# Kernel tuning notes

Hardware: AMD Instinct MI355X
Metric: run time of the kernel (lower is better)

Reference implementation:

```python
import jax, jax.numpy as jnp
import numpy as np

N, E, F = 50000, 1_600_000, 128
EPS = 1e-5
DATASET_NUM = 1.0


def _glorot(k, shape):
    lim = jnp.sqrt(6.0 / (shape[0] + shape[1]))
    return jax.random.uniform(k, shape, jnp.float32, -lim, lim)


def setup_inputs() -> dict:
    key = jax.random.key(0)
    ks = jax.random.split(key, 24)
    inp = {
        "x": jax.random.normal(ks[0], (N, F), jnp.float32),
        "noise": jax.random.normal(ks[1], (N, F), jnp.float32),
        "edge_index": jax.random.randint(ks[2], (2, E), 0, N, jnp.int64),
        # ChebConv K=2 weights: W0 (T_0 = x term), W1 (T_1 = L_hat x term)
        "W1_0": _glorot(ks[3], (F, 64)),  "W1_1": _glorot(ks[4], (F, 64)),  "b1": jnp.zeros((64,), jnp.float32),
        "g1": jnp.ones((64,), jnp.float32), "be1": jnp.zeros((64,), jnp.float32),
        "W2_0": _glorot(ks[5], (64, 16)), "W2_1": _glorot(ks[6], (64, 16)), "b2": jnp.zeros((16,), jnp.float32),
        "W3_0": _glorot(ks[7], (16, 64)), "W3_1": _glorot(ks[8], (16, 64)), "b3": jnp.zeros((64,), jnp.float32),
        "g3": jnp.ones((64,), jnp.float32), "be3": jnp.zeros((64,), jnp.float32),
        "W4_0": _glorot(ks[9], (64, F)),  "W4_1": _glorot(ks[10], (64, F)), "b4": jnp.zeros((F,), jnp.float32),
    }
    return inp


def reference(x, noise, edge_index, W1_0, W1_1, b1, g1, be1,
              W2_0, W2_1, b2, W3_0, W3_1, b3, g3, be3, W4_0, W4_1, b4):
    src, dst = edge_index[0], edge_index[1]
    n = x.shape[0]

    # train-mode noise injection: x + dataset_num * randn * x.mean()
    x = x + DATASET_NUM * noise * jnp.mean(x)

    # symmetric normalization; with lambda_max=2 the scaled Laplacian is -A_norm
    deg = jax.ops.segment_sum(jnp.ones_like(src, dtype=x.dtype), dst, num_segments=n)
    dinv = jnp.where(deg > 0, jax.lax.rsqrt(jnp.maximum(deg, 1.0)), 0.0)
    w_e = dinv[src] * dinv[dst]  # [E]

    def cheb(h, W0, W1, b):
        # T_0 = h ; T_1 = L_hat h = -A_norm h  (K=2 ChebConv)
        tx1 = -jax.ops.segment_sum(w_e[:, None] * h[src], dst, num_segments=n)
        return h @ W0 + tx1 @ W1 + b

    def bn(h, g, be):
        mu = jnp.mean(h, axis=0)
        var = jnp.mean((h - mu) ** 2, axis=0)
        return g * (h - mu) * jax.lax.rsqrt(var + EPS) + be

    h1 = jax.nn.relu(bn(cheb(x, W1_0, W1_1, b1), g1, be1))
    h2 = cheb(h1, W2_0, W2_1, b2)
    h3 = jax.nn.relu(bn(cheb(h2, W3_0, W3_1, b3), g3, be3))
    return cheb(h3, W4_0, W4_1, b4)
```

## Files before the change

### kernel.cpp

```cpp
#include <hip/hip_runtime.h>

#define NNODES 50000
#define NEDGES 1600000
#define FEAT   128
#define EPSV   1e-5f

__global__ __launch_bounds__(256) void sum_kernel(const float* __restrict__ x,
                                                  float* __restrict__ out, int n4) {
  const float4* x4 = (const float4*)x;
  float s = 0.f;
  for (int i = blockIdx.x * blockDim.x + threadIdx.x; i < n4; i += gridDim.x * blockDim.x) {
    float4 v = x4[i];
    s += v.x + v.y + v.z + v.w;
  }
  for (int off = 32; off > 0; off >>= 1) s += __shfl_down(s, off);
  __shared__ float ls[4];
  int wid = threadIdx.x >> 6;
  if ((threadIdx.x & 63) == 0) ls[wid] = s;
  __syncthreads();
  if (threadIdx.x == 0) atomicAdd(out, ls[0] + ls[1] + ls[2] + ls[3]);
}

__global__ __launch_bounds__(256) void noisy_kernel(const float* __restrict__ x,
                                                    const float* __restrict__ noise,
                                                    const float* __restrict__ sumv,
                                                    float* __restrict__ xn, int n4) {
  int i = blockIdx.x * blockDim.x + threadIdx.x;
  if (i >= n4) return;
  float mean = *sumv * (1.0f / (float)(NNODES * FEAT));
  float4 a = ((const float4*)x)[i];
  float4 b = ((const float4*)noise)[i];
  float4 o;
  o.x = a.x + b.x * mean; o.y = a.y + b.y * mean;
  o.z = a.z + b.z * mean; o.w = a.w + b.w * mean;
  ((float4*)xn)[i] = o;
}

__global__ __launch_bounds__(256) void degree_kernel(const int* __restrict__ ei,
                                                     int* __restrict__ degi, int ne) {
  int e = blockIdx.x * blockDim.x + threadIdx.x;
  if (e < ne) atomicAdd(&degi[ei[NEDGES + e]], 1);
}

__global__ __launch_bounds__(256) void dinv_kernel(const int* __restrict__ degi,
                                                   float* __restrict__ dinv, int n) {
  int i = blockIdx.x * blockDim.x + threadIdx.x;
  if (i < n) dinv[i] = (degi[i] > 0) ? rsqrtf((float)degi[i]) : 0.f;
}

__global__ __launch_bounds__(1024) void scan1_kernel(const int* __restrict__ cnt,
                                                     int* __restrict__ exc,
                                                     int* __restrict__ bsum, int n) {
  __shared__ int s[1024];
  int tid = threadIdx.x;
  int i = blockIdx.x * 1024 + tid;
  int v = (i < n) ? cnt[i] : 0;
  int val = v;
  s[tid] = v;
  __syncthreads();
  for (int off = 1; off < 1024; off <<= 1) {
    int t = (tid >= off) ? s[tid - off] : 0;
    __syncthreads();
    val += t;
    s[tid] = val;
    __syncthreads();
  }
  if (i < n) exc[i] = val - v;
  if (tid == 1023) bsum[blockIdx.x] = val;
}

__global__ __launch_bounds__(256) void scan2_kernel(int* __restrict__ bsum, int nb) {
  __shared__ int s[256];
  int tid = threadIdx.x;
  int v = (tid < nb) ? bsum[tid] : 0;
  int val = v;
  s[tid] = v;
  __syncthreads();
  for (int off = 1; off < 256; off <<= 1) {
    int t = (tid >= off) ? s[tid - off] : 0;
    __syncthreads();
    val += t;
    s[tid] = val;
    __syncthreads();
  }
  if (tid < nb) bsum[tid] = val - v;
}

__global__ __launch_bounds__(256) void scan3_kernel(int* __restrict__ row_ptr,
                                                    const int* __restrict__ bsum,
                                                    int* __restrict__ cursor, int n) {
  int i = blockIdx.x * blockDim.x + threadIdx.x;
  if (i < n) {
    int v = row_ptr[i] + bsum[i >> 10];
    row_ptr[i] = v;
    cursor[i] = v;
  } else if (i == n) {
    row_ptr[n] = NEDGES;
  }
}

__global__ __launch_bounds__(256) void csr_fill_kernel(const int* __restrict__ ei,
                                                       const float* __restrict__ dinv,
                                                       int* __restrict__ cursor,
                                                       int2* __restrict__ ep, int ne) {
  int e = blockIdx.x * blockDim.x + threadIdx.x;
  if (e >= ne) return;
  int s = ei[e];
  int d = ei[NEDGES + e];
  float w = dinv[s] * dinv[d];
  int pos = atomicAdd(&cursor[d], 1);
  ep[pos] = make_int2(s, __float_as_int(w));
}

template <int K, int NOUT, bool ROWCAT, bool BIAS>
__global__ __launch_bounds__(256) void gemm_kernel(const float* __restrict__ A1,
                                                   const float* __restrict__ A2,
                                                   const float* __restrict__ W0,
                                                   const float* __restrict__ W1,
                                                   const float* __restrict__ bias,
                                                   float* __restrict__ out, int n) {
  constexpr int TC  = NOUT / 4;
  constexpr int RG  = 256 / TC;
  constexpr int RPT = 4;
  constexpr int RPB = RG * RPT;
  constexpr int AP  = (K == 128) ? K : (K + 1);
  __shared__ float wl[K * NOUT];
  __shared__ float al[RPB * AP];
  const int tid = threadIdx.x;

  for (int i = tid; i < K * NOUT; i += 256) {
    int k = i / NOUT, j = i - k * NOUT;
    float v;
    if (ROWCAT) v = (k < K / 2) ? W0[k * NOUT + j] : W1[(k - K / 2) * NOUT + j];
    else        v = (j < NOUT / 2) ? W0[k * (NOUT / 2) + j] : W1[k * (NOUT / 2) + (j - NOUT / 2)];
    wl[i] = v;
  }
  const int row0 = blockIdx.x * RPB;
  for (int i = tid; i < RPB * K; i += 256) {
    int r = i / K, k = i - r * K;
    int gr = row0 + r;
    float v = 0.f;
    if (gr < n) {
      if (ROWCAT) v = (k < K / 2) ? A1[gr * (K / 2) + k] : A2[gr * (K / 2) + (k - K / 2)];
      else        v = A1[gr * K + k];
    }
    al[r * AP + k] = v;
  }
  __syncthreads();

  const int jt = (tid % TC) * 4;
  const int rbase = (tid / TC) * RPT;
  float acc[RPT][4] = {};
#pragma unroll 4
  for (int k = 0; k < K; ++k) {
    float4 w4 = *(const float4*)&wl[k * NOUT + jt];
#pragma unroll
    for (int rr = 0; rr < RPT; ++rr) {
      float a = al[(rbase + rr) * AP + k];
      acc[rr][0] = fmaf(a, w4.x, acc[rr][0]);
      acc[rr][1] = fmaf(a, w4.y, acc[rr][1]);
      acc[rr][2] = fmaf(a, w4.z, acc[rr][2]);
      acc[rr][3] = fmaf(a, w4.w, acc[rr][3]);
    }
  }
  float4 b4 = make_float4(0.f, 0.f, 0.f, 0.f);
  if (BIAS) b4 = *(const float4*)&bias[jt];
#pragma unroll
  for (int rr = 0; rr < RPT; ++rr) {
    int gr = row0 + rbase + rr;
    if (gr < n) {
      float4 o;
      o.x = acc[rr][0] + b4.x; o.y = acc[rr][1] + b4.y;
      o.z = acc[rr][2] + b4.z; o.w = acc[rr][3] + b4.w;
      *(float4*)&out[gr * NOUT + jt] = o;
    }
  }
}

template <int F, bool ADD>
__global__ __launch_bounds__(256) void spmm_kernel(const int* __restrict__ row_ptr,
                                                   const int2* __restrict__ ep,
                                                   const float* __restrict__ mat, int S, int OFF,
                                                   const float* __restrict__ bias,
                                                   float* __restrict__ out, int n) {
  constexpr int GP = 256 / F;
  const int f = threadIdx.x & (F - 1);
  const int g = threadIdx.x / F;
  const int node = blockIdx.x * GP + g;
  if (node >= n) return;
  const int beg = row_ptr[node];
  const int end = row_ptr[node + 1];
  float acc = 0.f;
  int e = beg;
  for (; e + 1 < end; e += 2) {
    int2 sw0 = ep[e];
    int2 sw1 = ep[e + 1];
    acc -= __int_as_float(sw0.y) * mat[sw0.x * S + OFF + f];
    acc -= __int_as_float(sw1.y) * mat[sw1.x * S + OFF + f];
  }
  if (e < end) {
    int2 sw = ep[e];
    acc -= __int_as_float(sw.y) * mat[sw.x * S + OFF + f];
  }
  float r = acc;
  if (ADD) r += mat[node * S + f] + bias[f];
  out[node * F + f] = r;
}

template <int F>
__global__ __launch_bounds__(256) void bn_stats_kernel(const float* __restrict__ z,
                                                       float* __restrict__ stats, int n) {
  __shared__ float s[2 * F];
  if (threadIdx.x < 2 * F) s[threadIdx.x] = 0.f;
  __syncthreads();
  constexpr int GP = 256 / F;
  const int f = threadIdx.x & (F - 1);
  const int g = threadIdx.x / F;
  float sum = 0.f, sq = 0.f;
  for (int r = blockIdx.x * GP + g; r < n; r += gridDim.x * GP) {
    float v = z[r * F + f];
    sum += v;
    sq += v * v;
  }
  atomicAdd(&s[f], sum);
  atomicAdd(&s[F + f], sq);
  __syncthreads();
  if (threadIdx.x < 2 * F) atomicAdd(&stats[threadIdx.x], s[threadIdx.x]);
}

template <int F>
__global__ __launch_bounds__(256) void bn_apply_kernel(float* __restrict__ z,
                                                       const float* __restrict__ stats,
                                                       const float* __restrict__ gw,
                                                       const float* __restrict__ be, int n) {
  const int idx = blockIdx.x * blockDim.x + threadIdx.x;
  if (idx >= n * F) return;
  const int f = idx & (F - 1);
  const float inv_n = 1.0f / (float)n;
  float mu = stats[f] * inv_n;
  float var = stats[F + f] * inv_n - mu * mu;
  float v = (z[idx] - mu) * rsqrtf(var + EPSV) * gw[f] + be[f];
  z[idx] = fmaxf(v, 0.f);
}

extern "C" void kernel_launch(void* const* d_in, const int* in_sizes, int n_in,
                              void* d_out, int out_size, void* d_ws, size_t ws_size,
                              hipStream_t stream) {
  const float* x     = (const float*)d_in[0];
  const float* noise = (const float*)d_in[1];
  const int*   ei    = (const int*)d_in[2];
  const float* W1_0 = (const float*)d_in[3];
  const float* W1_1 = (const float*)d_in[4];
  const float* b1   = (const float*)d_in[5];
  const float* g1   = (const float*)d_in[6];
  const float* be1  = (const float*)d_in[7];
  const float* W2_0 = (const float*)d_in[8];
  const float* W2_1 = (const float*)d_in[9];
  const float* b2   = (const float*)d_in[10];
  const float* W3_0 = (const float*)d_in[11];
  const float* W3_1 = (const float*)d_in[12];
  const float* b3   = (const float*)d_in[13];
  const float* g3   = (const float*)d_in[14];
  const float* be3  = (const float*)d_in[15];
  const float* W4_0 = (const float*)d_in[16];
  const float* W4_1 = (const float*)d_in[17];
  const float* b4   = (const float*)d_in[18];
  float* out = (float*)d_out;

  char* p = (char*)d_ws;
  size_t off = 0;
  auto alloc = [&](size_t b) -> void* {
    void* r = p + off;
    off += (b + 255) & ~(size_t)255;
    return r;
  };
  float* s_sum  = (float*)alloc(4);
  float* stats0 = (float*)alloc(2 * 64 * 4);
  float* stats1 = (float*)alloc(2 * 64 * 4);
  int*   degi   = (int*)alloc(sizeof(int) * NNODES);
  size_t zero_bytes = off;
  float* dinv    = (float*)alloc(sizeof(float) * NNODES);
  int*   row_ptr = (int*)alloc(sizeof(int) * (NNODES + 1));
  int*   bsum    = (int*)alloc(256 * sizeof(int));
  int*   cursor  = (int*)alloc(sizeof(int) * NNODES);
  int2*  ep      = (int2*)alloc(8ULL * NEDGES);
  float* big1    = (float*)alloc(4ULL * NNODES * FEAT);
  float* h1      = (float*)alloc(4ULL * NNODES * 64);

  float* big0 = out;
  float* xn   = big0;
  float* zz2  = big0;
  float* h2   = big0 + (size_t)NNODES * 32;
  float* agg3 = big0 + (size_t)NNODES * 48;
  float* zz1  = big1;
  float* h3   = big1;
  float* agg4 = big1 + (size_t)NNODES * 64;

  hipMemsetAsync(d_ws, 0, zero_bytes, stream);

  int n4 = NNODES * FEAT / 4;
  sum_kernel<<<2048, 256, 0, stream>>>(x, s_sum, n4);
  noisy_kernel<<<(n4 + 255) / 256, 256, 0, stream>>>(x, noise, s_sum, xn, n4);
  degree_kernel<<<(NEDGES + 255) / 256, 256, 0, stream>>>(ei, degi, NEDGES);
  dinv_kernel<<<(NNODES + 255) / 256, 256, 0, stream>>>(degi, dinv, NNODES);
  scan1_kernel<<<(NNODES + 1023) / 1024, 1024, 0, stream>>>(degi, row_ptr, bsum, NNODES);
  scan2_kernel<<<1, 256, 0, stream>>>(bsum, (NNODES + 1023) / 1024);
  scan3_kernel<<<(NNODES + 256) / 256, 256, 0, stream>>>(row_ptr, bsum, cursor, NNODES);
  csr_fill_kernel<<<(NEDGES + 255) / 256, 256, 0, stream>>>(ei, dinv, cursor, ep, NEDGES);

  gemm_kernel<128, 128, false, false><<<(NNODES + 31) / 32, 256, 0, stream>>>(
      xn, nullptr, W1_0, W1_1, nullptr, zz1, NNODES);
  spmm_kernel<64, true><<<(NNODES + 3) / 4, 256, 0, stream>>>(
      row_ptr, ep, zz1, 128, 64, b1, h1, NNODES);
  bn_stats_kernel<64><<<256, 256, 0, stream>>>(h1, stats0, NNODES);
  bn_apply_kernel<64><<<(NNODES * 64 + 255) / 256, 256, 0, stream>>>(h1, stats0, g1, be1, NNODES);

  gemm_kernel<64, 32, false, false><<<(NNODES + 127) / 128, 256, 0, stream>>>(
      h1, nullptr, W2_0, W2_1, nullptr, zz2, NNODES);
  spmm_kernel<16, true><<<(NNODES + 15) / 16, 256, 0, stream>>>(
      row_ptr, ep, zz2, 32, 16, b2, h2, NNODES);

  spmm_kernel<16, false><<<(NNODES + 15) / 16, 256, 0, stream>>>(
      row_ptr, ep, h2, 16, 0, nullptr, agg3, NNODES);
  gemm_kernel<32, 64, true, true><<<(NNODES + 63) / 64, 256, 0, stream>>>(
      h2, agg3, W3_0, W3_1, b3, h3, NNODES);
  bn_stats_kernel<64><<<256, 256, 0, stream>>>(h3, stats1, NNODES);
  bn_apply_kernel<64><<<(NNODES * 64 + 255) / 256, 256, 0, stream>>>(h3, stats1, g3, be3, NNODES);

  spmm_kernel<64, false><<<(NNODES + 3) / 4, 256, 0, stream>>>(
      row_ptr, ep, h3, 64, 0, nullptr, agg4, NNODES);
  gemm_kernel<128, 128, true, true><<<(NNODES + 31) / 32, 256, 0, stream>>>(
      h3, agg4, W4_0, W4_1, b4, out, NNODES);
}
```

Baseline: 755.6 us.

## Fuse noise, batchnorm stats and apply into GEMM/SpMM, vectorize SpMM gathers

Noise injection is folded into the first GEMM's A-tile load, removing a separate full-size write and read. BatchNorm statistics are accumulated in the epilogues of the SpMM and GEMM kernels, and the normalize-plus-ReLU step is applied lazily by consumers when they load their inputs. The separate stats and apply kernels are removed. The SpMM now has each lane gather a float4 with four independent accumulators, and the 128-wide GEMMs are split into two 64-column launches to cut shared memory per block. In exchange, the second-layer BN is recomputed for every gathered neighbour row, and the column split re-reads the A operand and re-applies noise in both launches.

```diff
diff --git a/kernel.cpp b/kernel.cpp
--- a/kernel.cpp
+++ b/kernel.cpp
@@ -4,6 +4,20 @@
 #define NEDGES 1600000
 #define FEAT   128
 #define EPSV   1e-5f
+
+__device__ __forceinline__ float4 f4fma(float w, float4 r, float4 a) {
+  a.x = fmaf(w, r.x, a.x); a.y = fmaf(w, r.y, a.y);
+  a.z = fmaf(w, r.z, a.z); a.w = fmaf(w, r.w, a.w);
+  return a;
+}
+__device__ __forceinline__ float4 f4bnrelu(float4 r, float4 s, float4 t) {
+  float4 o;
+  o.x = fmaxf(fmaf(r.x, s.x, t.x), 0.f);
+  o.y = fmaxf(fmaf(r.y, s.y, t.y), 0.f);
+  o.z = fmaxf(fmaf(r.z, s.z, t.z), 0.f);
+  o.w = fmaxf(fmaf(r.w, s.w, t.w), 0.f);
+  return o;
+}
 
 __global__ __launch_bounds__(256) void sum_kernel(const float* __restrict__ x,
                                                   float* __restrict__ out, int n4) {
@@ -19,21 +33,6 @@
   if ((threadIdx.x & 63) == 0) ls[wid] = s;
   __syncthreads();
   if (threadIdx.x == 0) atomicAdd(out, ls[0] + ls[1] + ls[2] + ls[3]);
-}
-
-__global__ __launch_bounds__(256) void noisy_kernel(const float* __restrict__ x,
-                                                    const float* __restrict__ noise,
-                                                    const float* __restrict__ sumv,
-                                                    float* __restrict__ xn, int n4) {
-  int i = blockIdx.x * blockDim.x + threadIdx.x;
-  if (i >= n4) return;
-  float mean = *sumv * (1.0f / (float)(NNODES * FEAT));
-  float4 a = ((const float4*)x)[i];
-  float4 b = ((const float4*)noise)[i];
-  float4 o;
-  o.x = a.x + b.x * mean; o.y = a.y + b.y * mean;
-  o.z = a.z + b.z * mean; o.w = a.w + b.w * mean;
-  ((float4*)xn)[i] = o;
 }
 
 __global__ __launch_bounds__(256) void degree_kernel(const int* __restrict__ ei,
@@ -112,27 +111,132 @@
   ep[pos] = make_int2(s, __float_as_int(w));
 }
 
-template <int K, int NOUT, bool ROWCAT, bool BIAS>
-__global__ __launch_bounds__(256) void gemm_kernel(const float* __restrict__ A1,
-                                                   const float* __restrict__ A2,
-                                                   const float* __restrict__ W0,
-                                                   const float* __restrict__ W1,
-                                                   const float* __restrict__ bias,
-                                                   float* __restrict__ out, int n) {
-  constexpr int TC  = NOUT / 4;
+template <int F, int S, int OFF, bool ADD, bool STATS, bool BNIN>
+__global__ __launch_bounds__(256) void spmm_kernel(
+    const int* __restrict__ row_ptr, const int2* __restrict__ ep,
+    const float* __restrict__ mat, const float* __restrict__ bias,
+    const float* __restrict__ stats_in, const float* __restrict__ gin,
+    const float* __restrict__ bein, float* __restrict__ stats_out,
+    float* __restrict__ out, int n) {
+  constexpr int LPN = F / 4;
+  constexpr int NPB = 256 / LPN;
+  __shared__ float sst[STATS ? 2 * F : 1];
+  if (STATS) {
+    if (threadIdx.x < 2 * F) sst[threadIdx.x] = 0.f;
+    __syncthreads();
+  }
+  const int lane = threadIdx.x & (LPN - 1);
+  const int g = threadIdx.x / LPN;
+  const int node = blockIdx.x * NPB + g;
+  const int f0 = lane * 4;
+  float4 scl = make_float4(0.f, 0.f, 0.f, 0.f), sht = scl;
+  if (BNIN) {
+    const float inv_n = 1.0f / (float)n;
+    float4 su = *(const float4*)&stats_in[f0];
+    float4 sq = *(const float4*)&stats_in[F + f0];
+    float4 gg = *(const float4*)&gin[f0];
+    float4 bb = *(const float4*)&bein[f0];
+    float mu;
+    mu = su.x * inv_n; scl.x = gg.x * rsqrtf(sq.x * inv_n - mu * mu + EPSV); sht.x = bb.x - mu * scl.x;
+    mu = su.y * inv_n; scl.y = gg.y * rsqrtf(sq.y * inv_n - mu * mu + EPSV); sht.y = bb.y - mu * scl.y;
+    mu = su.z * inv_n; scl.z = gg.z * rsqrtf(sq.z * inv_n - mu * mu + EPSV); sht.z = bb.z - mu * scl.z;
+    mu = su.w * inv_n; scl.w = gg.w * rsqrtf(sq.w * inv_n - mu * mu + EPSV); sht.w = bb.w - mu * scl.w;
+  }
+  if (node < n) {
+    const float* mb = mat + OFF + f0;
+    int e = row_ptr[node];
+    const int end = row_ptr[node + 1];
+    float4 a0 = make_float4(0.f, 0.f, 0.f, 0.f), a1 = a0, a2 = a0, a3 = a0;
+    for (; e + 3 < end; e += 4) {
+      int2 s0 = ep[e], s1 = ep[e + 1], s2 = ep[e + 2], s3 = ep[e + 3];
+      float4 r0 = *(const float4*)(mb + (size_t)s0.x * S);
+      float4 r1 = *(const float4*)(mb + (size_t)s1.x * S);
+      float4 r2 = *(const float4*)(mb + (size_t)s2.x * S);
+      float4 r3 = *(const float4*)(mb + (size_t)s3.x * S);
+      if (BNIN) {
+        r0 = f4bnrelu(r0, scl, sht); r1 = f4bnrelu(r1, scl, sht);
+        r2 = f4bnrelu(r2, scl, sht); r3 = f4bnrelu(r3, scl, sht);
+      }
+      a0 = f4fma(__int_as_float(s0.y), r0, a0);
+      a1 = f4fma(__int_as_float(s1.y), r1, a1);
+      a2 = f4fma(__int_as_float(s2.y), r2, a2);
+      a3 = f4fma(__int_as_float(s3.y), r3, a3);
+    }
+    for (; e < end; ++e) {
+      int2 s0 = ep[e];
+      float4 r0 = *(const float4*)(mb + (size_t)s0.x * S);
+      if (BNIN) r0 = f4bnrelu(r0, scl, sht);
+      a0 = f4fma(__int_as_float(s0.y), r0, a0);
+    }
+    float4 o;
+    o.x = (a0.x + a1.x) + (a2.x + a3.x);
+    o.y = (a0.y + a1.y) + (a2.y + a3.y);
+    o.z = (a0.z + a1.z) + (a2.z + a3.z);
+    o.w = (a0.w + a1.w) + (a2.w + a3.w);
+    if (ADD) {
+      float4 base = *(const float4*)&mat[(size_t)node * S + f0];
+      float4 b4 = *(const float4*)&bias[f0];
+      o.x = base.x + b4.x - o.x; o.y = base.y + b4.y - o.y;
+      o.z = base.z + b4.z - o.z; o.w = base.w + b4.w - o.w;
+    } else {
+      o.x = -o.x; o.y = -o.y; o.z = -o.z; o.w = -o.w;
+    }
+    *(float4*)&out[(size_t)node * F + f0] = o;
+    if (STATS) {
+      atomicAdd(&sst[f0 + 0], o.x); atomicAdd(&sst[F + f0 + 0], o.x * o.x);
+      atomicAdd(&sst[f0 + 1], o.y); atomicAdd(&sst[F + f0 + 1], o.y * o.y);
+      atomicAdd(&sst[f0 + 2], o.z); atomicAdd(&sst[F + f0 + 2], o.z * o.z);
+      atomicAdd(&sst[f0 + 3], o.w); atomicAdd(&sst[F + f0 + 3], o.w * o.w);
+    }
+  }
+  if (STATS) {
+    __syncthreads();
+    if (threadIdx.x < 2 * F) atomicAdd(&stats_out[threadIdx.x], sst[threadIdx.x]);
+  }
+}
+
+template <int K, int NB, int NT, bool ROWCAT, bool BIAS, bool BNIN, bool STATS, bool NOISE>
+__global__ __launch_bounds__(256) void gemm_kernel(
+    const float* __restrict__ A1, const float* __restrict__ A2,
+    const float* __restrict__ W0, const float* __restrict__ W1,
+    const float* __restrict__ bias, int col0,
+    const float* __restrict__ noise, const float* __restrict__ sumv,
+    const float* __restrict__ stats_in, const float* __restrict__ gin,
+    const float* __restrict__ bein, float* __restrict__ stats_out,
+    float* __restrict__ out, int n) {
+  constexpr int TC  = NB / 4;
   constexpr int RG  = 256 / TC;
   constexpr int RPT = 4;
   constexpr int RPB = RG * RPT;
   constexpr int AP  = (K == 128) ? K : (K + 1);
-  __shared__ float wl[K * NOUT];
+  constexpr int KB  = ROWCAT ? K / 2 : K;
+  __shared__ float wl[K * NB];
   __shared__ float al[RPB * AP];
+  __shared__ float sarr[BNIN ? KB : 1];
+  __shared__ float tarr[BNIN ? KB : 1];
+  __shared__ float sst[STATS ? 2 * NB : 1];
   const int tid = threadIdx.x;
-
-  for (int i = tid; i < K * NOUT; i += 256) {
-    int k = i / NOUT, j = i - k * NOUT;
+  if (STATS && tid < 2 * NB) sst[tid] = 0.f;
+  if (BNIN) {
+    const float inv_n = 1.0f / (float)n;
+    for (int f = tid; f < KB; f += 256) {
+      float mu = stats_in[f] * inv_n;
+      float var = stats_in[KB + f] * inv_n - mu * mu;
+      float s = gin[f] * rsqrtf(var + EPSV);
+      sarr[f] = s;
+      tarr[f] = bein[f] - mu * s;
+    }
+    __syncthreads();
+  }
+  float mean = 0.f;
+  if (NOISE) mean = sumv[0] * (1.0f / (float)(NNODES * FEAT));
+
+  for (int i = tid; i < K * NB; i += 256) {
+    int k = i / NB, j = i - k * NB;
+    int jg = col0 + j;
     float v;
-    if (ROWCAT) v = (k < K / 2) ? W0[k * NOUT + j] : W1[(k - K / 2) * NOUT + j];
-    else        v = (j < NOUT / 2) ? W0[k * (NOUT / 2) + j] : W1[k * (NOUT / 2) + (j - NOUT / 2)];
+    if (ROWCAT) v = (k < K / 2) ? W0[k * NT + jg] : W1[(k - K / 2) * NT + jg];
+    else        v = (jg < NT / 2) ? W0[k * (NT / 2) + jg] : W1[k * (NT / 2) + (jg - NT / 2)];
     wl[i] = v;
   }
   const int row0 = blockIdx.x * RPB;
@@ -141,8 +245,18 @@
     int gr = row0 + r;
     float v = 0.f;
     if (gr < n) {
-      if (ROWCAT) v = (k < K / 2) ? A1[gr * (K / 2) + k] : A2[gr * (K / 2) + (k - K / 2)];
-      else        v = A1[gr * K + k];
+      if (ROWCAT) {
+        if (k < K / 2) {
+          v = A1[(size_t)gr * (K / 2) + k];
+          if (BNIN) v = fmaxf(fmaf(v, sarr[k], tarr[k]), 0.f);
+        } else {
+          v = A2[(size_t)gr * (K / 2) + (k - K / 2)];
+        }
+      } else {
+        v = A1[(size_t)gr * K + k];
+        if (BNIN) v = fmaxf(fmaf(v, sarr[k], tarr[k]), 0.f);
+        if (NOISE) v = fmaf(noise[(size_t)gr * K + k], mean, v);
+      }
     }
     al[r * AP + k] = v;
   }
@@ -153,7 +267,7 @@
   float acc[RPT][4] = {};
 #pragma unroll 4
   for (int k = 0; k < K; ++k) {
-    float4 w4 = *(const float4*)&wl[k * NOUT + jt];
+    float4 w4 = *(const float4*)&wl[k * NB + jt];
 #pragma unroll
     for (int rr = 0; rr < RPT; ++rr) {
       float a = al[(rbase + rr) * AP + k];
@@ -164,83 +278,31 @@
     }
   }
   float4 b4 = make_float4(0.f, 0.f, 0.f, 0.f);
-  if (BIAS) b4 = *(const float4*)&bias[jt];
+  if (BIAS) b4 = *(const float4*)&bias[col0 + jt];
+  float sl[4] = {}, ql[4] = {};
 #pragma unroll
   for (int rr = 0; rr < RPT; ++rr) {
     int gr = row0 + rbase + rr;
     if (gr < n) {
-      float4 o;
-      o.x = acc[rr][0] + b4.x; o.y = acc[rr][1] + b4.y;
-      o.z = acc[rr][2] + b4.z; o.w = acc[rr][3] + b4.w;
-      *(float4*)&out[gr * NOUT + jt] = o;
-    }
-  }
-}
-
-template <int F, bool ADD>
-__global__ __launch_bounds__(256) void spmm_kernel(const int* __restrict__ row_ptr,
-                                                   const int2* __restrict__ ep,
-                                                   const float* __restrict__ mat, int S, int OFF,
-                                                   const float* __restrict__ bias,
-                                                   float* __restrict__ out, int n) {
-  constexpr int GP = 256 / F;
-  const int f = threadIdx.x & (F - 1);
-  const int g = threadIdx.x / F;
-  const int node = blockIdx.x * GP + g;
-  if (node >= n) return;
-  const int beg = row_ptr[node];
-  const int end = row_ptr[node + 1];
-  float acc = 0.f;
-  int e = beg;
-  for (; e + 1 < end; e += 2) {
-    int2 sw0 = ep[e];
-    int2 sw1 = ep[e + 1];
-    acc -= __int_as_float(sw0.y) * mat[sw0.x * S + OFF + f];
-    acc -= __int_as_float(sw1.y) * mat[sw1.x * S + OFF + f];
-  }
-  if (e < end) {
-    int2 sw = ep[e];
-    acc -= __int_as_float(sw.y) * mat[sw.x * S + OFF + f];
-  }
-  float r = acc;
-  if (ADD) r += mat[node * S + f] + bias[f];
-  out[node * F + f] = r;
-}
-
-template <int F>
-__global__ __launch_bounds__(256) void bn_stats_kernel(const float* __restrict__ z,
-                                                       float* __restrict__ stats, int n) {
-  __shared__ float s[2 * F];
-  if (threadIdx.x < 2 * F) s[threadIdx.x] = 0.f;
-  __syncthreads();
-  constexpr int GP = 256 / F;
-  const int f = threadIdx.x & (F - 1);
-  const int g = threadIdx.x / F;
-  float sum = 0.f, sq = 0.f;
-  for (int r = blockIdx.x * GP + g; r < n; r += gridDim.x * GP) {
-    float v = z[r * F + f];
-    sum += v;
-    sq += v * v;
-  }
-  atomicAdd(&s[f], sum);
-  atomicAdd(&s[F + f], sq);
-  __syncthreads();
-  if (threadIdx.x < 2 * F) atomicAdd(&stats[threadIdx.x], s[threadIdx.x]);
-}
-
-template <int F>
-__global__ __launch_bounds__(256) void bn_apply_kernel(float* __restrict__ z,
-                                                       const float* __restrict__ stats,
-                                                       const float* __restrict__ gw,
-                                                       const float* __restrict__ be, int n) {
-  const int idx = blockIdx.x * blockDim.x + threadIdx.x;
-  if (idx >= n * F) return;
-  const int f = idx & (F - 1);
-  const float inv_n = 1.0f / (float)n;
-  float mu = stats[f] * inv_n;
-  float var = stats[F + f] * inv_n - mu * mu;
-  float v = (z[idx] - mu) * rsqrtf(var + EPSV) * gw[f] + be[f];
-  z[idx] = fmaxf(v, 0.f);
+      float o0 = acc[rr][0] + b4.x, o1 = acc[rr][1] + b4.y;
+      float o2 = acc[rr][2] + b4.z, o3 = acc[rr][3] + b4.w;
+      float4 o = make_float4(o0, o1, o2, o3);
+      *(float4*)&out[(size_t)gr * NT + col0 + jt] = o;
+      if (STATS) {
+        sl[0] += o0; ql[0] += o0 * o0; sl[1] += o1; ql[1] += o1 * o1;
+        sl[2] += o2; ql[2] += o2 * o2; sl[3] += o3; ql[3] += o3 * o3;
+      }
+    }
+  }
+  if (STATS) {
+#pragma unroll
+    for (int j = 0; j < 4; ++j) {
+      atomicAdd(&sst[jt + j], sl[j]);
+      atomicAdd(&sst[NB + jt + j], ql[j]);
+    }
+    __syncthreads();
+    if (tid < 2 * NB) atomicAdd(&stats_out[tid], sst[tid]);
+  }
 }
 
 extern "C" void kernel_launch(void* const* d_in, const int* in_sizes, int n_in,
@@ -288,7 +350,6 @@
   float* h1      = (float*)alloc(4ULL * NNODES * 64);
 
   float* big0 = out;
-  float* xn   = big0;
   float* zz2  = big0;
   float* h2   = big0 + (size_t)NNODES * 32;
   float* agg3 = big0 + (size_t)NNODES * 48;
@@ -300,7 +361,6 @@
 
   int n4 = NNODES * FEAT / 4;
   sum_kernel<<<2048, 256, 0, stream>>>(x, s_sum, n4);
-  noisy_kernel<<<(n4 + 255) / 256, 256, 0, stream>>>(x, noise, s_sum, xn, n4);
   degree_kernel<<<(NEDGES + 255) / 256, 256, 0, stream>>>(ei, degi, NEDGES);
   dinv_kernel<<<(NNODES + 255) / 256, 256, 0, stream>>>(degi, dinv, NNODES);
   scan1_kernel<<<(NNODES + 1023) / 1024, 1024, 0, stream>>>(degi, row_ptr, bsum, NNODES);
@@ -308,27 +368,33 @@
   scan3_kernel<<<(NNODES + 256) / 256, 256, 0, stream>>>(row_ptr, bsum, cursor, NNODES);
   csr_fill_kernel<<<(NEDGES + 255) / 256, 256, 0, stream>>>(ei, dinv, cursor, ep, NEDGES);
 
-  gemm_kernel<128, 128, false, false><<<(NNODES + 31) / 32, 256, 0, stream>>>(
-      xn, nullptr, W1_0, W1_1, nullptr, zz1, NNODES);
-  spmm_kernel<64, true><<<(NNODES + 3) / 4, 256, 0, stream>>>(
-      row_ptr, ep, zz1, 128, 64, b1, h1, NNODES);
-  bn_stats_kernel<64><<<256, 256, 0, stream>>>(h1, stats0, NNODES);
-  bn_apply_kernel<64><<<(NNODES * 64 + 255) / 256, 256, 0, stream>>>(h1, stats0, g1, be1, NNODES);
-
-  gemm_kernel<64, 32, false, false><<<(NNODES + 127) / 128, 256, 0, stream>>>(
-      h1, nullptr, W2_0, W2_1, nullptr, zz2, NNODES);
-  spmm_kernel<16, true><<<(NNODES + 15) / 16, 256, 0, stream>>>(
-      row_ptr, ep, zz2, 32, 16, b2, h2, NNODES);
-
-  spmm_kernel<16, false><<<(NNODES + 15) / 16, 256, 0, stream>>>(
-      row_ptr, ep, h2, 16, 0, nullptr, agg3, NNODES);
-  gemm_kernel<32, 64, true, true><<<(NNODES + 63) / 64, 256, 0, stream>>>(
-      h2, agg3, W3_0, W3_1, b3, h3, NNODES);
-  bn_stats_kernel<64><<<256, 256, 0, stream>>>(h3, stats1, NNODES);
-  bn_apply_kernel<64><<<(NNODES * 64 + 255) / 256, 256, 0, stream>>>(h3, stats1, g3, be3, NNODES);
-
-  spmm_kernel<64, false><<<(NNODES + 3) / 4, 256, 0, stream>>>(
-      row_ptr, ep, h3, 64, 0, nullptr, agg4, NNODES);
-  gemm_kernel<128, 128, true, true><<<(NNODES + 31) / 32, 256, 0, stream>>>(
-      h3, agg4, W4_0, W4_1, b4, out, NNODES);
-}
+  gemm_kernel<128, 64, 128, false, false, false, false, true>
+      <<<(NNODES + 63) / 64, 256, 0, stream>>>(x, nullptr, W1_0, W1_1, nullptr, 0,
+          noise, s_sum, nullptr, nullptr, nullptr, nullptr, zz1, NNODES);
+  gemm_kernel<128, 64, 128, false, false, false, false, true>
+      <<<(NNODES + 63) / 64, 256, 0, stream>>>(x, nullptr, W1_0, W1_1, nullptr, 64,
+          noise, s_sum, nullptr, nullptr, nullptr, nullptr, zz1, NNODES);
+  spmm_kernel<64, 128, 64, true, true, false><<<(NNODES + 15) / 16, 256, 0, stream>>>(
+      row_ptr, ep, zz1, b1, nullptr, nullptr, nullptr, stats0, h1, NNODES);
+
+  gemm_kernel<64, 32, 32, false, false, true, false, false>
+      <<<(NNODES + 127) / 128, 256, 0, stream>>>(h1, nullptr, W2_0, W2_1, nullptr, 0,
+          nullptr, nullptr, stats0, g1, be1, nullptr, zz2, NNODES);
+  spmm_kernel<16, 32, 16, true, false, false><<<(NNODES + 63) / 64, 256, 0, stream>>>(
+      row_ptr, ep, zz2, b2, nullptr, nullptr, nullptr, nullptr, h2, NNODES);
+
+  spmm_kernel<16, 16, 0, false, false, false><<<(NNODES + 63) / 64, 256, 0, stream>>>(
+      row_ptr, ep, h2, nullptr, nullptr, nullptr, nullptr, nullptr, agg3, NNODES);
+  gemm_kernel<32, 64, 64, true, true, false, true, false>
+      <<<(NNODES + 63) / 64, 256, 0, stream>>>(h2, agg3, W3_0, W3_1, b3, 0,
+          nullptr, nullptr, nullptr, nullptr, nullptr, stats1, h3, NNODES);
+
+  spmm_kernel<64, 64, 0, false, false, true><<<(NNODES + 15) / 16, 256, 0, stream>>>(
+      row_ptr, ep, h3, nullptr, stats1, g3, be3, nullptr, agg4, NNODES);
+  gemm_kernel<128, 64, 128, true, true, true, false, false>
+      <<<(NNODES + 63) / 64, 256, 0, stream>>>(h3, agg4, W4_0, W4_1, b4, 0,
+          nullptr, nullptr, stats1, g3, be3, nullptr, out, NNODES);
+  gemm_kernel<128, 64, 128, true, true, true, false, false>
+      <<<(NNODES + 63) / 64, 256, 0, stream>>>(h3, agg4, W4_0, W4_1, b4, 64,
+          nullptr, nullptr, stats1, g3, be3, nullptr, out, NNODES);
+}
```

Result: faster. 736.8 us (-2.5%).
